# Kernel tuning notes

Hardware: AMD Instinct MI355X
Metric: run time of the kernel (lower is better)

## Reference

```python
import jax, jax.numpy as jnp
import numpy as np

NUM_HEADS = 16
D_MODEL = 1024
D_K = D_MODEL // NUM_HEADS


def setup_inputs() -> dict:
    key = jax.random.key(0)
    ks = jax.random.split(key, 11)
    B, S = 2, 2048
    s = 1.0 / np.sqrt(D_MODEL)
    return {
        "Q": jax.random.normal(ks[0], (B, S, D_MODEL), jnp.float32),
        "K": jax.random.normal(ks[1], (B, S, D_MODEL), jnp.float32),
        "V": jax.random.normal(ks[2], (B, S, D_MODEL), jnp.float32),
        "Wq": jax.random.normal(ks[3], (D_MODEL, D_MODEL), jnp.float32) * s,
        "bq": jnp.zeros((D_MODEL,), jnp.float32),
        "Wk": jax.random.normal(ks[4], (D_MODEL, D_MODEL), jnp.float32) * s,
        "bk": jnp.zeros((D_MODEL,), jnp.float32),
        "Wv": jax.random.normal(ks[5], (D_MODEL, D_MODEL), jnp.float32) * s,
        "bv": jnp.zeros((D_MODEL,), jnp.float32),
        "Wo": jax.random.normal(ks[6], (D_MODEL, D_MODEL), jnp.float32) * s,
        "bo": jnp.zeros((D_MODEL,), jnp.float32),
    }


def _split_heads(x):
    B, S, _ = x.shape
    return x.reshape(B, S, NUM_HEADS, D_K).transpose(0, 2, 1, 3)  # (B,H,S,Dk)


def reference(Q, K, V, Wq, bq, Wk, bk, Wv, bv, Wo, bo):
    q = _split_heads(Q @ Wq + bq)
    k = _split_heads(K @ Wk + bk)
    v = _split_heads(V @ Wv + bv)
    scores = jnp.einsum("bhqd,bhkd->bhqk", q, k) / jnp.sqrt(jnp.asarray(D_K, q.dtype))
    attn = jax.nn.softmax(scores, axis=-1)
    out = jnp.einsum("bhqk,bhkd->bhqd", attn, v)  # (B,H,S,Dk)
    B, H, S, Dk = out.shape
    combined = out.transpose(0, 2, 1, 3).reshape(B, S, H * Dk)
    return combined @ Wo + bo
```

## Files before the change

### kernel.cpp

```cpp
#include <hip/hip_runtime.h>
#include <stdint.h>

#define DM   1024
#define NH   16
#define DKH  64
#define SEQ  2048
#define NB   2

typedef __attribute__((ext_vector_type(8))) short  frag8;
typedef __attribute__((ext_vector_type(4))) short  frag4;
typedef __attribute__((ext_vector_type(4))) short  short4v;
typedef __attribute__((ext_vector_type(8))) short  short8v;
typedef __attribute__((ext_vector_type(4))) float  f32x4;

__device__ __forceinline__ unsigned short f2bf(float x){
  unsigned u = __float_as_uint(x);
  u += 0x7fffu + ((u >> 16) & 1u);
  return (unsigned short)(u >> 16);
}

__device__ __forceinline__ float dev_exp2(float x){
  return __builtin_amdgcn_exp2f(x);
}

#define GLOAD16(GP, LP) __builtin_amdgcn_global_load_lds( \
    (__attribute__((address_space(1))) void*)(GP), \
    (__attribute__((address_space(3))) void*)(LP), 16, 0, 0)

#define LDSFENCE() do{ asm volatile("" ::: "memory"); \
                       __builtin_amdgcn_sched_barrier(0); }while(0)



__global__ __launch_bounds__(256) void cast_qkv(const float* __restrict__ Q,
                                                const float* __restrict__ K,
                                                const float* __restrict__ V,
                                                short* __restrict__ dst){
  const int z = blockIdx.z;
  const float* src = (z == 0) ? Q : (z == 1 ? K : V);
  const int i = (blockIdx.x * 256 + threadIdx.x) * 4;
  float4 f = *(const float4*)(src + i);
  short4v s;
  s.x = (short)f2bf(f.x); s.y = (short)f2bf(f.y);
  s.z = (short)f2bf(f.z); s.w = (short)f2bf(f.w);
  *(short4v*)(dst + (long)z * (SEQ*NB*DM) + i) = s;
}

__global__ __launch_bounds__(256) void wtrans(const float* __restrict__ Wq,
                                              const float* __restrict__ Wk,
                                              const float* __restrict__ Wv,
                                              const float* __restrict__ Wo,
                                              short* __restrict__ wt){
  const int z = blockIdx.z;
  const float* W = (z == 0) ? Wq : (z == 1 ? Wk : (z == 2 ? Wv : Wo));
  short* out = wt + (long)z * (DM*DM);
  __shared__ float t[32][33];
  const int n0 = blockIdx.x * 32, k0 = blockIdx.y * 32;
  const int c = threadIdx.x & 31, r0 = threadIdx.x >> 5;
#pragma unroll
  for (int i = 0; i < 4; ++i){
    int r = r0 + i * 8;
    t[r][c] = W[(k0 + r) * DM + n0 + c];
  }
  __syncthreads();
#pragma unroll
  for (int i = 0; i < 4; ++i){
    int r = r0 + i * 8;
    out[(n0 + r) * DM + k0 + c] = (short)f2bf(t[c][r]);
  }
}

__device__ __forceinline__ void store_out(short* p, float v){ *p = (short)f2bf(v); }
__device__ __forceinline__ void store_out(float* p, float v){ *p = v; }

template<typename OT>
__global__ __launch_bounds__(256) void gemm_bt(const short* __restrict__ Abase, long Astride,
                                               const short* __restrict__ Btbase, long Btstride,
                                               const float* __restrict__ bias0,
                                               const float* __restrict__ bias1,
                                               const float* __restrict__ bias2,
                                               OT* __restrict__ Cbase, long Cstride,
                                               float qscale){
  const int z = blockIdx.z;
  const short* A  = Abase + (long)z * Astride;
  const short* Bt = Btbase + (long)z * Btstride;
  OT* C = Cbase + (long)z * Cstride;
  const float* bias = (z == 0) ? bias0 : (z == 1 ? bias1 : bias2);
  const float scale = (z == 0) ? qscale : 1.0f;
  const int KD = DM, ND = DM;

  __shared__ __align__(16) short As[2][128 * 64];
  __shared__ __align__(16) short Bs[2][128 * 64];

  const int tid = threadIdx.x;
  const int w = tid >> 6, lane = tid & 63, l15 = lane & 15, quad = lane >> 4;
  const int wy = w >> 1, wx = w & 1;
  const int bm = blockIdx.x * 128, bn = blockIdx.y * 128;
  const int lrow = lane >> 3;
  const int lcolsw = (((lane & 7) ^ lrow) & 7) * 8;

  f32x4 acc[4][4] = {};

#define GSTAGE(KT, BSEL) do{                                                    \
  _Pragma("unroll")                                                             \
  for (int i_ = 0; i_ < 4; ++i_){                                               \
    int j_ = w * 4 + i_;                                                        \
    GLOAD16(A  + (bm + j_ * 8 + lrow) * KD + (KT) * 64 + lcolsw,                \
            &As[BSEL][j_ * 512]);                                               \
    GLOAD16(Bt + (bn + j_ * 8 + lrow) * KD + (KT) * 64 + lcolsw,                \
            &Bs[BSEL][j_ * 512]);                                               \
  } }while(0)

#define GCOMPUTE(BS) do{                                                        \
  _Pragma("unroll") for (int ks = 0; ks < 2; ++ks){                             \
    frag8 af[4], bf_[4];                                                        \
    _Pragma("unroll") for (int mt = 0; mt < 4; ++mt)                            \
      af[mt] = *(const frag8*)&As[BS][(wy * 64 + mt * 16 + l15) * 64 +          \
                                      (((ks * 4 + quad) ^ (l15 & 7)) * 8)];     \
    _Pragma("unroll") for (int nt = 0; nt < 4; ++nt)                            \
      bf_[nt] = *(const frag8*)&Bs[BS][(wx * 64 + nt * 16 + l15) * 64 +         \
                                       (((ks * 4 + quad) ^ (l15 & 7)) * 8)];    \
    _Pragma("unroll") for (int mt = 0; mt < 4; ++mt)                            \
      _Pragma("unroll") for (int nt = 0; nt < 4; ++nt)                          \
        acc[mt][nt] = __builtin_amdgcn_mfma_f32_16x16x32_bf16(                  \
            af[mt], bf_[nt], acc[mt][nt], 0, 0, 0);                             \
  } }while(0)

  GSTAGE(0, 0);
  for (int t = 0; t < KD / 64 - 1; ++t){
    GSTAGE(t + 1, (t + 1) & 1);
    asm volatile("s_waitcnt vmcnt(8)" ::: "memory");
    __builtin_amdgcn_s_barrier();
    LDSFENCE();
    GCOMPUTE(t & 1);
    asm volatile("s_waitcnt lgkmcnt(0)" ::: "memory");
    __builtin_amdgcn_sched_barrier(0);
    __builtin_amdgcn_s_barrier();
  }
  asm volatile("s_waitcnt vmcnt(0)" ::: "memory");
  __builtin_amdgcn_s_barrier();
  LDSFENCE();
  GCOMPUTE(1);

#undef GSTAGE
#undef GCOMPUTE

#pragma unroll
  for (int mt = 0; mt < 4; ++mt){
#pragma unroll
    for (int r = 0; r < 4; ++r){
      int m = bm + wy * 64 + mt * 16 + quad * 4 + r;
#pragma unroll
      for (int nt = 0; nt < 4; ++nt){
        int n = bn + wx * 64 + nt * 16 + l15;
        float v = (acc[mt][nt][r] + bias[n]) * scale;
        store_out(&C[(long)m * ND + n], v);
      }
    }
  }
}

template<typename OT>
__global__ __launch_bounds__(256) void gemm64_bt(const short* __restrict__ A,
                                                 const short* __restrict__ Bt,
                                                 const float* __restrict__ bias,
                                                 OT* __restrict__ C,
                                                 float scale){
  const int KD = DM, ND = DM;
  __shared__ __align__(16) short As[2][64 * 64];
  __shared__ __align__(16) short Bs[2][128 * 64];
  const int tid = threadIdx.x;
  const int w = tid >> 6, lane = tid & 63, l15 = lane & 15, quad = lane >> 4;
  const int wy = w >> 1, wx = w & 1;
  const int bm = blockIdx.x * 64, bn = blockIdx.y * 128;
  const int lrow = lane >> 3;
  const int lcolsw = (((lane & 7) ^ lrow) & 7) * 8;
  f32x4 acc[2][4] = {};

#define GSTAGE64(KT, BSEL) do{                                                  \
  _Pragma("unroll")                                                             \
  for (int i_ = 0; i_ < 2; ++i_){                                               \
    int j_ = w * 2 + i_;                                                        \
    GLOAD16(A + (bm + j_ * 8 + lrow) * KD + (KT) * 64 + lcolsw,                 \
            &As[BSEL][j_ * 512]);                                               \
  }                                                                             \
  _Pragma("unroll")                                                             \
  for (int i_ = 0; i_ < 4; ++i_){                                               \
    int j_ = w * 4 + i_;                                                        \
    GLOAD16(Bt + (bn + j_ * 8 + lrow) * KD + (KT) * 64 + lcolsw,                \
            &Bs[BSEL][j_ * 512]);                                               \
  } }while(0)

#define GCOMPUTE64(BS) do{                                                      \
  _Pragma("unroll") for (int ks = 0; ks < 2; ++ks){                             \
    frag8 af[2], bf_[4];                                                        \
    _Pragma("unroll") for (int mt = 0; mt < 2; ++mt)                            \
      af[mt] = *(const frag8*)&As[BS][(wy * 32 + mt * 16 + l15) * 64 +          \
                                      (((ks * 4 + quad) ^ (l15 & 7)) * 8)];     \
    _Pragma("unroll") for (int nt = 0; nt < 4; ++nt)                            \
      bf_[nt] = *(const frag8*)&Bs[BS][(wx * 64 + nt * 16 + l15) * 64 +         \
                                       (((ks * 4 + quad) ^ (l15 & 7)) * 8)];    \
    _Pragma("unroll") for (int mt = 0; mt < 2; ++mt)                            \
      _Pragma("unroll") for (int nt = 0; nt < 4; ++nt)                          \
        acc[mt][nt] = __builtin_amdgcn_mfma_f32_16x16x32_bf16(                  \
            af[mt], bf_[nt], acc[mt][nt], 0, 0, 0);                             \
  } }while(0)

  GSTAGE64(0, 0);
  for (int t = 0; t < KD / 64 - 1; ++t){
    GSTAGE64(t + 1, (t + 1) & 1);
    asm volatile("s_waitcnt vmcnt(6)" ::: "memory");
    __builtin_amdgcn_s_barrier();
    LDSFENCE();
    GCOMPUTE64(t & 1);
    asm volatile("s_waitcnt lgkmcnt(0)" ::: "memory");
    __builtin_amdgcn_sched_barrier(0);
    __builtin_amdgcn_s_barrier();
  }
  asm volatile("s_waitcnt vmcnt(0)" ::: "memory");
  __builtin_amdgcn_s_barrier();
  LDSFENCE();
  GCOMPUTE64(1);

#undef GSTAGE64
#undef GCOMPUTE64

#pragma unroll
  for (int mt = 0; mt < 2; ++mt){
#pragma unroll
    for (int r = 0; r < 4; ++r){
      int m = bm + wy * 32 + mt * 16 + quad * 4 + r;
#pragma unroll
      for (int nt = 0; nt < 4; ++nt){
        int n = bn + wx * 64 + nt * 16 + l15;
        store_out(&C[(long)m * ND + n], (acc[mt][nt][r] + bias[n]) * scale);
      }
    }
  }
}

__global__ __launch_bounds__(256) void vtrans(const short* __restrict__ v,
                                              short* __restrict__ vt){
  const int bh = blockIdx.y;
  const int b = bh >> 4, h = bh & 15;
  const int s0 = blockIdx.x * 64;
  __shared__ short tT[64][66];
  const short* vb = v + ((long)(b * SEQ + s0)) * DM + h * DKH;
  for (int j = threadIdx.x; j < 512; j += 256){
    int row = j >> 3, off = (j & 7) * 8;
    short8v d = *(const short8v*)(vb + row * DM + off);
#pragma unroll
    for (int e = 0; e < 8; ++e) tT[off + e][row] = d[e];
  }
  __syncthreads();
  short* out = vt + (long)bh * (DKH * SEQ) + s0;
  for (int j = threadIdx.x; j < 512; j += 256){
    int dr = j >> 3, soff = (j & 7) * 8;
    short8v o;
#pragma unroll
    for (int e = 0; e < 8; ++e) o[e] = tT[dr][soff + e];
    *(short8v*)(out + dr * SEQ + soff) = o;
  }
}

__global__ __launch_bounds__(256) void flash(const short* __restrict__ q,
                                             const short* __restrict__ k,
                                             const short* __restrict__ vt,
                                             short* __restrict__ comb){
  const int bh = blockIdx.y;
  const int b = bh >> 4, h = bh & 15;
  const int q0 = blockIdx.x * 128;
  const int tid = threadIdx.x;
  const int w = tid >> 6, lane = tid & 63, l15 = lane & 15, quad = lane >> 4;

  __shared__ __align__(16) short Ks[3][64 * 64];
  __shared__ __align__(16) short Vs[3][64 * 64];

  frag8 aq[2][2];
  const short* qb = q + ((long)(b * SEQ + q0 + w * 32)) * DM + h * DKH;
#pragma unroll
  for (int mt = 0; mt < 2; ++mt)
#pragma unroll
    for (int ks = 0; ks < 2; ++ks)
      aq[mt][ks] = *(const frag8*)(qb + (mt * 16 + l15) * DM + ks * 32 + quad * 8);

  frag4 ones4;
#pragma unroll
  for (int e = 0; e < 4; ++e) ones4[e] = (short)0x3F80;

  f32x4 O[2][4] = {};
  f32x4 Lacc[2] = {{0.f,0.f,0.f,0.f},{0.f,0.f,0.f,0.f}};

  const short* kb  = k + ((long)b * SEQ) * DM + h * DKH;
  const short* vtb = vt + (long)bh * (DKH * SEQ);
  const int lrow8 = lane >> 3;
  const int lcolsw = (((lane & 7) ^ lrow8) & 7) * 8;

#define STAGE(KT, BSEL) do{                                                     \
  _Pragma("unroll")                                                             \
  for (int i_ = 0; i_ < 2; ++i_){                                               \
    int jj_ = w * 2 + i_;                                                       \
    GLOAD16(kb + ((KT) * 64 + jj_ * 8 + lrow8) * DM + lcolsw,                   \
            &Ks[BSEL][jj_ * 512]);                                              \
    GLOAD16(vtb + (jj_ * 8 + lrow8) * SEQ + (KT) * 64 + lcolsw,                 \
            &Vs[BSEL][jj_ * 512]);                                              \
  } }while(0)

#define COMPUTE(BS) do{                                                         \
  __builtin_amdgcn_s_setprio(1);                                                \
  f32x4 scT[2][4];                                                              \
  _Pragma("unroll") for (int mt = 0; mt < 2; ++mt)                              \
    _Pragma("unroll") for (int nt = 0; nt < 4; ++nt)                            \
      scT[mt][nt] = (f32x4){0.f, 0.f, 0.f, 0.f};                                \
  _Pragma("unroll") for (int ks = 0; ks < 2; ++ks){                             \
    _Pragma("unroll") for (int nt = 0; nt < 4; ++nt){                           \
      frag8 ak = *(const frag8*)&Ks[BS][(nt * 16 + l15) * 64 +                  \
                                        (((ks * 4 + quad) ^ (l15 & 7)) * 8)];   \
      _Pragma("unroll") for (int mt = 0; mt < 2; ++mt)                          \
        scT[mt][nt] = __builtin_amdgcn_mfma_f32_16x16x32_bf16(                  \
            ak, aq[mt][ks], scT[mt][nt], 0, 0, 0);                              \
    }                                                                           \
  }                                                                             \
  frag4 ap[2][4];                                                               \
  _Pragma("unroll") for (int mt = 0; mt < 2; ++mt)                              \
    _Pragma("unroll") for (int nt = 0; nt < 4; ++nt){                           \
      _Pragma("unroll") for (int r = 0; r < 4; ++r){                            \
        float e = dev_exp2(scT[mt][nt][r]);                                     \
        ap[mt][nt][r] = (short)((__float_as_uint(e) + 0x8000u) >> 16);          \
      }                                                                         \
    }                                                                           \
  _Pragma("unroll") for (int nt = 0; nt < 4; ++nt){                             \
    _Pragma("unroll") for (int dt = 0; dt < 4; ++dt){                           \
      frag4 bv4 = *(const frag4*)&Vs[BS][(dt * 16 + l15) * 64 +                 \
                                   (((nt * 2 + (quad >> 1)) ^ (l15 & 7)) * 8) + \
                                   (quad & 1) * 4];                             \
      _Pragma("unroll") for (int mt = 0; mt < 2; ++mt)                          \
        O[mt][dt] = __builtin_amdgcn_mfma_f32_16x16x16bf16_1k(                  \
            ap[mt][nt], bv4, O[mt][dt], 0, 0, 0);                               \
    }                                                                           \
    _Pragma("unroll") for (int mt = 0; mt < 2; ++mt)                            \
      Lacc[mt] = __builtin_amdgcn_mfma_f32_16x16x16bf16_1k(                     \
          ap[mt][nt], ones4, Lacc[mt], 0, 0, 0);                                \
  }                                                                             \
  __builtin_amdgcn_s_setprio(0);                                                \
}while(0)

#define ITER(KT, BC, BSNEXT) do{                                                \
  STAGE((KT) + 2, BSNEXT);                                                      \
  asm volatile("s_waitcnt vmcnt(8)" ::: "memory");                              \
  __builtin_amdgcn_s_barrier();                                                 \
  LDSFENCE();                                                                   \
  COMPUTE(BC);                                                                  \
  asm volatile("s_waitcnt lgkmcnt(0)" ::: "memory");                            \
  __builtin_amdgcn_sched_barrier(0);                                            \
  __builtin_amdgcn_s_barrier();                                                 \
}while(0)

  STAGE(0, 0);
  STAGE(1, 1);
  for (int kt = 0; kt < SEQ / 64 - 2; kt += 3){
    ITER(kt,     0, 2);
    ITER(kt + 1, 1, 0);
    ITER(kt + 2, 2, 1);
  }
  asm volatile("s_waitcnt vmcnt(4)" ::: "memory");
  __builtin_amdgcn_s_barrier();
  LDSFENCE();
  COMPUTE(0);
  asm volatile("s_waitcnt vmcnt(0)" ::: "memory");
  __builtin_amdgcn_s_barrier();
  LDSFENCE();
  COMPUTE(1);

#undef ITER
#undef COMPUTE
#undef STAGE

  short* ob = comb + ((long)(b * SEQ + q0 + w * 32)) * DM + h * DKH;
#pragma unroll
  for (int mt = 0; mt < 2; ++mt){
#pragma unroll
    for (int r = 0; r < 4; ++r){
      float inv = 1.f / Lacc[mt][r];
#pragma unroll
      for (int nt = 0; nt < 4; ++nt)
        ob[(mt * 16 + quad * 4 + r) * DM + nt * 16 + l15] = (short)f2bf(O[mt][nt][r] * inv);
    }
  }
}

extern "C" void kernel_launch(void* const* d_in, const int* in_sizes, int n_in,
                              void* d_out, int out_size, void* d_ws, size_t ws_size,
                              hipStream_t stream){
  const float* Q  = (const float*)d_in[0];
  const float* K  = (const float*)d_in[1];
  const float* V  = (const float*)d_in[2];
  const float* Wq = (const float*)d_in[3];
  const float* bq = (const float*)d_in[4];
  const float* Wk = (const float*)d_in[5];
  const float* bk = (const float*)d_in[6];
  const float* Wv = (const float*)d_in[7];
  const float* bv = (const float*)d_in[8];
  const float* Wo = (const float*)d_in[9];
  const float* bo = (const float*)d_in[10];
  float* out = (float*)d_out;

  const long TEN = (long)NB * SEQ * DM;
  const long WEL = (long)DM * DM;
  short* ws   = (short*)d_ws;
  short* xc   = ws;
  short* wt   = xc + 3 * TEN;
  short* qkv  = wt + 4 * WEL;
  short* vtr  = qkv + 3 * TEN;
  short* comb = vtr + TEN;

  cast_qkv<<<dim3(4096, 1, 3), 256, 0, stream>>>(Q, K, V, xc);
  wtrans<<<dim3(32, 32, 4), 256, 0, stream>>>(Wq, Wk, Wv, Wo, wt);
  gemm_bt<short><<<dim3(32, 8, 3), 256, 0, stream>>>(xc, TEN, wt, WEL, bq, bk, bv,
                                                     qkv, TEN, 0.125f * 1.44269504f);
  vtrans<<<dim3(32, 32), 256, 0, stream>>>(qkv + 2 * TEN, vtr);
  flash<<<dim3(16, 32), 256, 0, stream>>>(qkv, qkv + TEN, vtr, comb);
  gemm64_bt<float><<<dim3(64, 8), 256, 0, stream>>>(comb, wt + 3 * WEL, bo, out, 1.0f);
  (void)in_sizes; (void)n_in; (void)out_size; (void)ws_size;
}
```

Before: 233.7 us.

## Use 16x16x32 bf16 MFMA for PV and row-sum by permuting K rows

Switches the P·V and row-sum accumulations in the attention kernel from 16x16x16 to 16x16x32 bf16 MFMA instructions, halving the instruction count for that stage. To make the score accumulator layout match the wider A operand, K rows are loaded into LDS in a permuted order, so two adjacent score tiles pack into one 8-element fragment. V is read with 8-wide LDS loads instead of 4-wide. Correctness depends on the row permutation exactly matching the K-index mapping of the wider MFMA.

```diff
diff --git a/kernel.cpp b/kernel.cpp
--- a/kernel.cpp
+++ b/kernel.cpp
@@ -284,9 +284,9 @@
     for (int ks = 0; ks < 2; ++ks)
       aq[mt][ks] = *(const frag8*)(qb + (mt * 16 + l15) * DM + ks * 32 + quad * 8);
 
-  frag4 ones4;
-#pragma unroll
-  for (int e = 0; e < 4; ++e) ones4[e] = (short)0x3F80;
+  frag8 ones8;
+#pragma unroll
+  for (int e = 0; e < 8; ++e) ones8[e] = (short)0x3F80;
 
   f32x4 O[2][4] = {};
   f32x4 Lacc[2] = {{0.f,0.f,0.f,0.f},{0.f,0.f,0.f,0.f}};
@@ -300,8 +300,9 @@
   _Pragma("unroll")                                                             \
   for (int i_ = 0; i_ < 2; ++i_){                                               \
     int jj_ = w * 2 + i_;                                                       \
-    GLOAD16(kb + ((KT) * 64 + jj_ * 8 + lrow8) * DM + lcolsw,                   \
-            &Ks[BSEL][jj_ * 512]);                                              \
+    int kr_ = 32 * (jj_ >> 2) + 8 * ((jj_ * 2 + (lrow8 >> 2)) & 3)              \
+            + 4 * ((jj_ >> 1) & 1) + (lrow8 & 3);                               \
+    GLOAD16(kb  + ((KT) * 64 + kr_) * DM + lcolsw,        &Ks[BSEL][jj_ * 512]);\
     GLOAD16(vtb + (jj_ * 8 + lrow8) * SEQ + (KT) * 64 + lcolsw,                 \
             &Vs[BSEL][jj_ * 512]);                                              \
   } }while(0)
@@ -321,26 +322,28 @@
             ak, aq[mt][ks], scT[mt][nt], 0, 0, 0);                              \
     }                                                                           \
   }                                                                             \
-  frag4 ap[2][4];                                                               \
+  frag8 ap8[2][2];                                                              \
   _Pragma("unroll") for (int mt = 0; mt < 2; ++mt)                              \
-    _Pragma("unroll") for (int nt = 0; nt < 4; ++nt){                           \
-      _Pragma("unroll") for (int r = 0; r < 4; ++r){                            \
-        float e = dev_exp2(scT[mt][nt][r]);                                     \
-        ap[mt][nt][r] = (short)((__float_as_uint(e) + 0x8000u) >> 16);          \
-      }                                                                         \
+    _Pragma("unroll") for (int c2 = 0; c2 < 2; ++c2){                           \
+      frag8 p8;                                                                 \
+      _Pragma("unroll") for (int hf = 0; hf < 2; ++hf)                          \
+        _Pragma("unroll") for (int r = 0; r < 4; ++r){                          \
+          float e = dev_exp2(scT[mt][2 * c2 + hf][r]);                          \
+          p8[hf * 4 + r] = (short)((__float_as_uint(e) + 0x8000u) >> 16);       \
+        }                                                                       \
+      ap8[mt][c2] = p8;                                                         \
     }                                                                           \
-  _Pragma("unroll") for (int nt = 0; nt < 4; ++nt){                             \
+  _Pragma("unroll") for (int c2 = 0; c2 < 2; ++c2){                             \
     _Pragma("unroll") for (int dt = 0; dt < 4; ++dt){                           \
-      frag4 bv4 = *(const frag4*)&Vs[BS][(dt * 16 + l15) * 64 +                 \
-                                   (((nt * 2 + (quad >> 1)) ^ (l15 & 7)) * 8) + \
-                                   (quad & 1) * 4];                             \
+      frag8 bv8 = *(const frag8*)&Vs[BS][(dt * 16 + l15) * 64 +                 \
+                                         (((c2 * 4 + quad) ^ (l15 & 7)) * 8)];  \
       _Pragma("unroll") for (int mt = 0; mt < 2; ++mt)                          \
-        O[mt][dt] = __builtin_amdgcn_mfma_f32_16x16x16bf16_1k(                  \
-            ap[mt][nt], bv4, O[mt][dt], 0, 0, 0);                               \
+        O[mt][dt] = __builtin_amdgcn_mfma_f32_16x16x32_bf16(                    \
+            ap8[mt][c2], bv8, O[mt][dt], 0, 0, 0);                              \
     }                                                                           \
     _Pragma("unroll") for (int mt = 0; mt < 2; ++mt)                            \
-      Lacc[mt] = __builtin_amdgcn_mfma_f32_16x16x16bf16_1k(                     \
-          ap[mt][nt], ones4, Lacc[mt], 0, 0, 0);                                \
+      Lacc[mt] = __builtin_amdgcn_mfma_f32_16x16x32_bf16(                       \
+          ap8[mt][c2], ones8, Lacc[mt], 0, 0, 0);                               \
   }                                                                             \
   __builtin_amdgcn_s_setprio(0);                                                \
 }while(0)
@@ -383,8 +386,8 @@
     for (int r = 0; r < 4; ++r){
       float inv = 1.f / Lacc[mt][r];
 #pragma unroll
-      for (int nt = 0; nt < 4; ++nt)
-        ob[(mt * 16 + quad * 4 + r) * DM + nt * 16 + l15] = (short)f2bf(O[mt][nt][r] * inv);
+      for (int dt = 0; dt < 4; ++dt)
+        ob[(mt * 16 + quad * 4 + r) * DM + dt * 16 + l15] = (short)f2bf(O[mt][dt][r] * inv);
     }
   }
 }
```

After: 224.3 us. -4.0%, faster.
